# Optimization experiments

Hardware: AMD Instinct MI355X
Metric: run time of the kernel (lower is better)

The kernel has to match this reference:

```python
import jax, jax.numpy as jnp
import numpy as np

H = 16        # num_heads
NB = 64       # n_buckets
NH = 6        # n_hyperplanes = log2(NB)


def setup_inputs() -> dict:
    key = jax.random.key(0)
    k = jax.random.split(key, 6)
    E = 1024
    B, S = 2, 2048
    return {
        "x": jax.random.normal(k[0], (B, S, E), jnp.float32),
        "Wq": jax.random.normal(k[1], (E, E), jnp.float32) * (E ** -0.5),
        "bq": jax.random.normal(k[2], (E,), jnp.float32) * 0.02,
        "Wv": jax.random.normal(k[3], (E, E), jnp.float32) * (E ** -0.5),
        "bv": jax.random.normal(k[4], (E,), jnp.float32) * 0.02,
        "hyperplanes": jax.random.normal(k[5], (E // H + 1, NH), jnp.float32),
    }


def reference(x, Wq, bq, Wv, bv, hyperplanes):
    B, S, E = x.shape
    Dh = E // H
    # projections (torch Linear: x @ W.T + b)
    q = (x @ Wq.T + bq).reshape(B, S, H, Dh)
    v = (x @ Wv.T + bv).reshape(B, S, H, Dh)

    # LSH buckets from q: append a ones column, sign-project onto hyperplanes
    qa = jnp.concatenate([q, jnp.ones((B, S, H, 1), q.dtype)], axis=-1)  # [B,S,H,Dh+1]
    proj = jnp.einsum('bshe,en->bshn', qa, hyperplanes)
    bits = (proj >= 0).astype(jnp.int32)
    buckets = jnp.einsum('bshn,n->bsh', bits, 2 ** jnp.arange(NH, dtype=jnp.int32))  # [B,S,H]
    b_hs = buckets.transpose(0, 2, 1)  # [B,H,S]

    q = q.transpose(0, 2, 1, 3)  # [B,H,S,Dh]
    v = v.transpose(0, 2, 1, 3)

    # The original sums, over all NB buckets i, of (q with bucket-i tokens zeroed)
    # times its transpose. Closed form of that sum:
    #   sum_i (1-d[bs,i])(1-d[bt,i]) = NB - 2 + [bs == bt]
    scores = jnp.einsum('bhsd,bhtd->bhst', q, q) / jnp.sqrt(jnp.float32(E))
    same = (b_hs[:, :, :, None] == b_hs[:, :, None, :]).astype(scores.dtype)
    coeff = (NB - 2) + same
    attn = jax.nn.softmax(scores * coeff, axis=-1)  # [B,H,S,S]

    out = jnp.einsum('bhst,bhtd->bhsd', attn, v)
    return out.transpose(0, 2, 1, 3).reshape(B, S, E)
```

## Files before the change

### kernel.cpp

```cpp
#include <hip/hip_runtime.h>


typedef short short8 __attribute__((ext_vector_type(8)));
typedef float f32x4 __attribute__((ext_vector_type(4)));
typedef unsigned short us4 __attribute__((ext_vector_type(4)));

__device__ __forceinline__ float bff(unsigned short h) {
    return __uint_as_float(((unsigned int)h) << 16);
}
__device__ __forceinline__ unsigned short f2bf(float f) {
    unsigned int u = __float_as_uint(f);
    u += 0x7fffu + ((u >> 16) & 1u);
    return (unsigned short)(u >> 16);
}

__device__ __forceinline__ void glds16(const unsigned short* g, unsigned short* l) {
    __builtin_amdgcn_global_load_lds(
        (const __attribute__((address_space(1))) unsigned int*)g,
        (__attribute__((address_space(3))) unsigned int*)l, 16, 0, 0);
}

__global__ __launch_bounds__(256) void split_all(
    const float* __restrict__ x, const float* __restrict__ Wq,
    const float* __restrict__ Wv,
    unsigned short* __restrict__ xh, unsigned short* __restrict__ xl,
    unsigned short* __restrict__ Wqh, unsigned short* __restrict__ Wql,
    unsigned short* __restrict__ Wvh)
{
    const int blk = blockIdx.x;
    const float* in;
    unsigned short *hi, *lo;
    int idx;
    if (blk < 4096) {
        idx = blk * 256 + threadIdx.x; in = x; hi = xh; lo = xl;
    } else if (blk < 5120) {
        idx = (blk - 4096) * 256 + threadIdx.x; in = Wq; hi = Wqh; lo = Wql;
    } else {
        idx = (blk - 5120) * 256 + threadIdx.x; in = Wv; hi = Wvh; lo = nullptr;
    }
    const float4 v = ((const float4*)in)[idx];
    us4 h;
    h.x = f2bf(v.x); h.y = f2bf(v.y); h.z = f2bf(v.z); h.w = f2bf(v.w);
    ((us4*)hi)[idx] = h;
    if (lo) {
        us4 l;
        l.x = f2bf(v.x - bff(h.x)); l.y = f2bf(v.y - bff(h.y));
        l.z = f2bf(v.z - bff(h.z)); l.w = f2bf(v.w - bff(h.w));
        ((us4*)lo)[idx] = l;
    }
}

__global__ __launch_bounds__(256, 1) void gemm_qv(
    const unsigned short* __restrict__ xh, const unsigned short* __restrict__ xl,
    const unsigned short* __restrict__ wqh, const unsigned short* __restrict__ wql,
    const unsigned short* __restrict__ wvh,
    const float* __restrict__ bq, const float* __restrict__ bv,
    float* __restrict__ Qf, unsigned short* __restrict__ Qb,
    unsigned short* __restrict__ Qlo, unsigned short* __restrict__ Vt)
{
    __shared__ unsigned short Ah[128 * 64], Al[128 * 64];
    __shared__ unsigned short Bh[128 * 64], Bl[128 * 64];

    const int tid = threadIdx.x;
    const int w = tid >> 6, lane = tid & 63;
    const int i = lane & 15, qd = lane >> 4;
    const int l8 = lane >> 3, j = lane & 7;
    const int nw = w * 32;
    const int blk = blockIdx.x;
    const bool isq = blk < 256;

    f32x4 acc[8][2];
#pragma unroll
    for (int a = 0; a < 8; ++a)
#pragma unroll
        for (int b2 = 0; b2 < 2; ++b2) acc[a][b2] = f32x4{0.f, 0.f, 0.f, 0.f};

    const int gro = ((j ^ l8) << 3);

    if (isq) {
        const int m0 = (blk >> 3) * 128;
        const int n0 = (blk & 7) * 128;
        for (int k0 = 0; k0 < 1024; k0 += 64) {
            __syncthreads();
#pragma unroll
            for (int c = 0; c < 4; ++c) {
                const int r = w * 32 + c * 8;
                const size_t gx = (size_t)(m0 + r + l8) * 1024 + k0 + gro;
                const size_t gw = (size_t)(n0 + r + l8) * 1024 + k0 + gro;
                glds16(xh + gx, &Ah[r * 64]);
                glds16(xl + gx, &Al[r * 64]);
                glds16(wqh + gw, &Bh[r * 64]);
                glds16(wql + gw, &Bl[r * 64]);
            }
            __syncthreads();
#pragma unroll
            for (int kc = 0; kc < 2; ++kc) {
                const int ch = (((kc * 4 + qd) ^ (i & 7)) << 3);
                short8 ah[8], al[8], bh2[2], bl2[2];
#pragma unroll
                for (int mm = 0; mm < 8; ++mm) {
                    ah[mm] = *(const short8*)&Ah[(mm * 16 + i) * 64 + ch];
                    al[mm] = *(const short8*)&Al[(mm * 16 + i) * 64 + ch];
                }
#pragma unroll
                for (int nn = 0; nn < 2; ++nn) {
                    bh2[nn] = *(const short8*)&Bh[(nw + nn * 16 + i) * 64 + ch];
                    bl2[nn] = *(const short8*)&Bl[(nw + nn * 16 + i) * 64 + ch];
                }
#pragma unroll
                for (int mm = 0; mm < 8; ++mm)
#pragma unroll
                    for (int nn = 0; nn < 2; ++nn) {
                        acc[mm][nn] = __builtin_amdgcn_mfma_f32_16x16x32_bf16(
                            ah[mm], bh2[nn], acc[mm][nn], 0, 0, 0);
                        acc[mm][nn] = __builtin_amdgcn_mfma_f32_16x16x32_bf16(
                            al[mm], bh2[nn], acc[mm][nn], 0, 0, 0);
                        acc[mm][nn] = __builtin_amdgcn_mfma_f32_16x16x32_bf16(
                            ah[mm], bl2[nn], acc[mm][nn], 0, 0, 0);
                    }
            }
        }
#pragma unroll
        for (int mm = 0; mm < 8; ++mm)
#pragma unroll
            for (int nn = 0; nn < 2; ++nn)
#pragma unroll
                for (int rr = 0; rr < 4; ++rr) {
                    const int row = m0 + mm * 16 + qd * 4 + rr;
                    const int col = n0 + nw + nn * 16 + i;
                    const float v = acc[mm][nn][rr] + bq[col];
                    Qf[(size_t)row * 1024 + col] = v;
                    const unsigned short hs = f2bf(v);
                    const float lo = v - bff(hs);
                    const int b = row >> 11, s = row & 2047;
                    const int hh = col >> 6, d = col & 63;
                    const size_t oi = ((size_t)((b << 4) + hh) * 2048 + s) * 64 + d;
                    Qb[oi] = hs;
                    Qlo[oi] = f2bf(lo);
                }
    } else {
        const int b2 = blk - 256;
        const int m0 = (b2 & 7) * 128;
        const int n0 = (b2 >> 3) * 128;
        for (int k0 = 0; k0 < 1024; k0 += 64) {
            __syncthreads();
#pragma unroll
            for (int c = 0; c < 4; ++c) {
                const int r = w * 32 + c * 8;
                glds16(wvh + (size_t)(m0 + r + l8) * 1024 + k0 + gro, &Ah[r * 64]);
                glds16(xh + (size_t)(n0 + r + l8) * 1024 + k0 + gro, &Bh[r * 64]);
            }
            __syncthreads();
#pragma unroll
            for (int kc = 0; kc < 2; ++kc) {
                const int ch = (((kc * 4 + qd) ^ (i & 7)) << 3);
                short8 af[8], bf2[2];
#pragma unroll
                for (int mm = 0; mm < 8; ++mm)
                    af[mm] = *(const short8*)&Ah[(mm * 16 + i) * 64 + ch];
#pragma unroll
                for (int nn = 0; nn < 2; ++nn)
                    bf2[nn] = *(const short8*)&Bh[(nw + nn * 16 + i) * 64 + ch];
#pragma unroll
                for (int mm = 0; mm < 8; ++mm)
#pragma unroll
                    for (int nn = 0; nn < 2; ++nn)
                        acc[mm][nn] = __builtin_amdgcn_mfma_f32_16x16x32_bf16(
                            af[mm], bf2[nn], acc[mm][nn], 0, 0, 0);
            }
        }
#pragma unroll
        for (int mm = 0; mm < 8; ++mm)
#pragma unroll
            for (int nn = 0; nn < 2; ++nn)
#pragma unroll
                for (int rr = 0; rr < 4; ++rr) {
                    const int rch = m0 + mm * 16 + qd * 4 + rr;
                    const int tok = n0 + nw + nn * 16 + i;
                    const float v = acc[mm][nn][rr] + bv[rch];
                    const int b = tok >> 11, s = tok & 2047;
                    Vt[((size_t)(b * 1024 + rch)) * 2048 + s] = f2bf(v);
                }
    }
}

__global__ __launch_bounds__(256) void bucket_kernel(
    const float* __restrict__ Qf, const float* __restrict__ hp,
    int* __restrict__ buckets, float* __restrict__ rown)
{
    __shared__ float hpl[65 * 6];
    const int tid = threadIdx.x;
    if (tid < 65 * 6) hpl[tid] = hp[tid];
    __syncthreads();

    const int idx = blockIdx.x * 256 + tid;
    const int m = idx >> 4, h = idx & 15;
    const float4* q4 = (const float4*)(Qf + (size_t)m * 1024 + h * 64);

    float pj[6];
    float nrm = 0.f;
#pragma unroll
    for (int n = 0; n < 6; ++n) pj[n] = hpl[64 * 6 + n];
    for (int d4 = 0; d4 < 16; ++d4) {
        const float4 qv = q4[d4];
        nrm = fmaf(qv.x, qv.x, nrm); nrm = fmaf(qv.y, qv.y, nrm);
        nrm = fmaf(qv.z, qv.z, nrm); nrm = fmaf(qv.w, qv.w, nrm);
#pragma unroll
        for (int n = 0; n < 6; ++n) {
            pj[n] = fmaf(qv.x, hpl[(d4 * 4 + 0) * 6 + n], pj[n]);
            pj[n] = fmaf(qv.y, hpl[(d4 * 4 + 1) * 6 + n], pj[n]);
            pj[n] = fmaf(qv.z, hpl[(d4 * 4 + 2) * 6 + n], pj[n]);
            pj[n] = fmaf(qv.w, hpl[(d4 * 4 + 3) * 6 + n], pj[n]);
        }
    }
    int bkt = 0;
#pragma unroll
    for (int n = 0; n < 6; ++n) bkt |= (pj[n] >= 0.f) << n;
    const int off = ((m >> 11) * 16 + h) * 2048 + (m & 2047);
    buckets[off] = bkt;
    rown[off] = nrm;
}

__global__ __launch_bounds__(256, 2) void attn_kernel(
    const unsigned short* __restrict__ Qb, const unsigned short* __restrict__ Qlo,
    const unsigned short* __restrict__ Vt, const int* __restrict__ bks,
    const float* __restrict__ rown, float* __restrict__ out)
{
    __shared__ unsigned short Khi[2][64 * 64];
    __shared__ unsigned short Klo[2][64 * 64];
    __shared__ unsigned short Vs[2][64 * 64];
    __shared__ unsigned short P[4][16 * 64];
    __shared__ float smax[4];

    const int tid = threadIdx.x;
    const int w = tid >> 6, lane = tid & 63;
    const int i = lane & 15, qd = lane >> 4;
    const int l8 = lane >> 3, j = lane & 7;
    const int bh = blockIdx.x;
    const int qbase = blockIdx.y * 128 + w * 32;

    const unsigned short* Qh = Qb + (size_t)bh * 2048 * 64;
    const unsigned short* Ql = Qlo + (size_t)bh * 2048 * 64;
    const unsigned short* Vb = Vt + (size_t)bh * 64 * 2048;
    const int* bk = bks + bh * 2048;
    const float* rnh = rown + bh * 2048;
    unsigned short* Pw = &P[w][0];

    float lm = 0.f;
    for (int t = tid; t < 2048; t += 256) lm = fmaxf(lm, rnh[t]);
#pragma unroll
    for (int msk = 1; msk < 64; msk <<= 1) lm = fmaxf(lm, __shfl_xor(lm, msk));
    if (lane == 0) smax[w] = lm;
    __syncthreads();
    const float sqM = sqrtf(fmaxf(fmaxf(smax[0], smax[1]),
                                  fmaxf(smax[2], smax[3])));

    float m2row[2][4], lrun[2][4];
    int qbr[2][4];
#pragma unroll
    for (int ms = 0; ms < 2; ++ms)
#pragma unroll
        for (int r = 0; r < 4; ++r) {
            const int row = qbase + ms * 16 + qd * 4 + r;
            m2row[ms][r] = 2.84030586f * sqrtf(rnh[row]) * sqM + 0.72134754f;
            qbr[ms][r] = bk[row];
            lrun[ms][r] = 0.f;
        }

    short8 aqh0[2], aqh1[2], aql0[2], aql1[2];
#pragma unroll
    for (int ms = 0; ms < 2; ++ms) {
        const unsigned short* qp = Qh + (size_t)(qbase + ms * 16 + i) * 64 + qd * 8;
        const unsigned short* lp = Ql + (size_t)(qbase + ms * 16 + i) * 64 + qd * 8;
        aqh0[ms] = *(const short8*)qp; aqh1[ms] = *(const short8*)(qp + 32);
        aql0[ms] = *(const short8*)lp; aql1[ms] = *(const short8*)(lp + 32);
    }

    f32x4 o[2][4];
#pragma unroll
    for (int ms = 0; ms < 2; ++ms)
#pragma unroll
        for (int d = 0; d < 4; ++d) o[ms][d] = f32x4{0.f, 0.f, 0.f, 0.f};

    const int swz = ((j ^ l8) << 3);

#pragma unroll
    for (int c2 = 0; c2 < 2; ++c2) {
        const int r = w * 16 + c2 * 8 + l8;
        glds16(Qh + (size_t)r * 64 + swz, &Khi[0][w * 1024 + c2 * 512]);
        glds16(Ql + (size_t)r * 64 + swz, &Klo[0][w * 1024 + c2 * 512]);
        glds16(Vb + (size_t)r * 2048 + swz, &Vs[0][w * 1024 + c2 * 512]);
    }

    for (int it = 0; it < 32; ++it) {
        const int t0 = it * 64;
        const int cur = it & 1;
        __syncthreads();
        if (it < 31) {
            const int t0n = t0 + 64;
            const int nxt = cur ^ 1;
#pragma unroll
            for (int c2 = 0; c2 < 2; ++c2) {
                const int r = w * 16 + c2 * 8 + l8;
                glds16(Qh + (size_t)(t0n + r) * 64 + swz, &Khi[nxt][w * 1024 + c2 * 512]);
                glds16(Ql + (size_t)(t0n + r) * 64 + swz, &Klo[nxt][w * 1024 + c2 * 512]);
                glds16(Vb + (size_t)r * 2048 + t0n + swz, &Vs[nxt][w * 1024 + c2 * 512]);
            }
        }

        f32x4 s[2][4];
        int kb[4];
#pragma unroll
        for (int sub = 0; sub < 4; ++sub) {
            const int kr = sub * 16 + i;
            const int sw = i & 7;
            const short8 bh0 = *(const short8*)&Khi[cur][kr * 64 + ((qd ^ sw) << 3)];
            const short8 bh1 = *(const short8*)&Khi[cur][kr * 64 + (((qd + 4) ^ sw) << 3)];
            const short8 bl0 = *(const short8*)&Klo[cur][kr * 64 + ((qd ^ sw) << 3)];
            const short8 bl1 = *(const short8*)&Klo[cur][kr * 64 + (((qd + 4) ^ sw) << 3)];
            kb[sub] = bk[t0 + kr];
#pragma unroll
            for (int ms = 0; ms < 2; ++ms) {
                f32x4 t = f32x4{0.f, 0.f, 0.f, 0.f};
                t = __builtin_amdgcn_mfma_f32_16x16x32_bf16(aqh0[ms], bh0, t, 0, 0, 0);
                t = __builtin_amdgcn_mfma_f32_16x16x32_bf16(aqh1[ms], bh1, t, 0, 0, 0);
                t = __builtin_amdgcn_mfma_f32_16x16x32_bf16(aql0[ms], bh0, t, 0, 0, 0);
                t = __builtin_amdgcn_mfma_f32_16x16x32_bf16(aql1[ms], bh1, t, 0, 0, 0);
                t = __builtin_amdgcn_mfma_f32_16x16x32_bf16(aqh0[ms], bl0, t, 0, 0, 0);
                t = __builtin_amdgcn_mfma_f32_16x16x32_bf16(aqh1[ms], bl1, t, 0, 0, 0);
                s[ms][sub] = t;
            }
        }

        short8 vb0[4], vb1[4];
#pragma unroll
        for (int dsub = 0; dsub < 4; ++dsub) {
            const int dr = dsub * 16 + i;
            const int sw = i & 7;
            vb0[dsub] = *(const short8*)&Vs[cur][dr * 64 + ((qd ^ sw) << 3)];
            vb1[dsub] = *(const short8*)&Vs[cur][dr * 64 + (((qd + 4) ^ sw) << 3)];
        }

#pragma unroll
        for (int ms = 0; ms < 2; ++ms) {
#pragma unroll
            for (int sub = 0; sub < 4; ++sub)
#pragma unroll
                for (int r = 0; r < 4; ++r) {
                    const float c2f = (kb[sub] == qbr[ms][r]) ? 2.84030586f
                                                              : 2.79522164f;
                    const float p = exp2f(fmaf(s[ms][sub][r], c2f, -m2row[ms][r]));
                    lrun[ms][r] += p;
                    const unsigned int pu = __float_as_uint(p);
                    const int row = qd * 4 + r, col = sub * 16 + i;
                    Pw[row * 64 + (((col >> 3) ^ (row & 7)) << 3) + (col & 7)] =
                        (unsigned short)(pu >> 16);
                }
            const short8 pa0 = *(const short8*)&Pw[i * 64 + ((qd ^ (i & 7)) << 3)];
            const short8 pa1 = *(const short8*)&Pw[i * 64 + (((qd + 4) ^ (i & 7)) << 3)];
#pragma unroll
            for (int dsub = 0; dsub < 4; ++dsub) {
                o[ms][dsub] = __builtin_amdgcn_mfma_f32_16x16x32_bf16(
                    pa0, vb0[dsub], o[ms][dsub], 0, 0, 0);
                o[ms][dsub] = __builtin_amdgcn_mfma_f32_16x16x32_bf16(
                    pa1, vb1[dsub], o[ms][dsub], 0, 0, 0);
            }
        }
    }

#pragma unroll
    for (int ms = 0; ms < 2; ++ms)
#pragma unroll
        for (int r = 0; r < 4; ++r) {
#pragma unroll
            for (int msk = 1; msk < 16; msk <<= 1)
                lrun[ms][r] += __shfl_xor(lrun[ms][r], msk);
        }
    const int b = bh >> 4, h = bh & 15;
#pragma unroll
    for (int ms = 0; ms < 2; ++ms)
#pragma unroll
        for (int dsub = 0; dsub < 4; ++dsub)
#pragma unroll
            for (int r = 0; r < 4; ++r) {
                const float v = o[ms][dsub][r] / lrun[ms][r];
                const int srow = qbase + ms * 16 + qd * 4 + r;
                out[((size_t)(b * 2048 + srow)) * 1024 + h * 64 + dsub * 16 + i] = v;
            }
}

extern "C" void kernel_launch(void* const* d_in, const int* in_sizes, int n_in,
                              void* d_out, int out_size, void* d_ws, size_t ws_size,
                              hipStream_t stream)
{
    const float* x  = (const float*)d_in[0];
    const float* Wq = (const float*)d_in[1];
    const float* bq = (const float*)d_in[2];
    const float* Wv = (const float*)d_in[3];
    const float* bv = (const float*)d_in[4];
    const float* hp = (const float*)d_in[5];
    float* out = (float*)d_out;

    char* ws = (char*)d_ws;
    const size_t MB = (size_t)1 << 20;
    unsigned short* xh  = (unsigned short*)(ws);
    unsigned short* xl  = (unsigned short*)(ws + 8 * MB);
    unsigned short* Wqh = (unsigned short*)(ws + 16 * MB);
    unsigned short* Wql = (unsigned short*)(ws + 18 * MB);
    unsigned short* Wvh = (unsigned short*)(ws + 20 * MB);
    unsigned short* Qb  = (unsigned short*)(ws + 22 * MB);
    unsigned short* Qlo = (unsigned short*)(ws + 30 * MB);
    unsigned short* Vt  = (unsigned short*)(ws + 38 * MB);
    float*          Qf  = (float*)(ws + 46 * MB);
    int*        buckets = (int*)(ws + 62 * MB);
    float*         rown = (float*)(ws + 62 * MB + 256 * 1024);

    split_all<<<dim3(6144), 256, 0, stream>>>(x, Wq, Wv, xh, xl, Wqh, Wql, Wvh);
    gemm_qv<<<dim3(512), 256, 0, stream>>>(xh, xl, Wqh, Wql, Wvh, bq, bv,
                                           Qf, Qb, Qlo, Vt);
    bucket_kernel<<<dim3(256), 256, 0, stream>>>(Qf, hp, buckets, rown);
    attn_kernel<<<dim3(32, 16), 256, 0, stream>>>(Qb, Qlo, Vt, buckets, rown, out);
}
```

Measured before the change: 229.5 us.

## Shrink attention tile to 16 rows per wave and drop double buffering

Each wave in the attention kernel now handles 16 query rows instead of 32, and the grid doubles to 32x32 blocks. The K/V LDS tiles become single-buffered with two barriers per iteration, and launch bounds rise to 4 blocks per CU. The aim is more resident waves and lower register and LDS use so the scheduler can hide latency. The cost is that each K/V tile loaded is reused across half as many query rows, which doubles global and LDS traffic, and the copy of the next tile no longer overlaps compute.

```diff
diff --git a/kernel.cpp b/kernel.cpp
--- a/kernel.cpp
+++ b/kernel.cpp
@@ -221,14 +221,14 @@
     rown[off] = nrm;
 }
 
-__global__ __launch_bounds__(256, 2) void attn_kernel(
+__global__ __launch_bounds__(256, 4) void attn_kernel(
     const unsigned short* __restrict__ Qb, const unsigned short* __restrict__ Qlo,
     const unsigned short* __restrict__ Vt, const int* __restrict__ bks,
     const float* __restrict__ rown, float* __restrict__ out)
 {
-    __shared__ unsigned short Khi[2][64 * 64];
-    __shared__ unsigned short Klo[2][64 * 64];
-    __shared__ unsigned short Vs[2][64 * 64];
+    __shared__ unsigned short Khi[64 * 64];
+    __shared__ unsigned short Klo[64 * 64];
+    __shared__ unsigned short Vs[64 * 64];
     __shared__ unsigned short P[4][16 * 64];
     __shared__ float smax[4];
 
@@ -237,7 +237,7 @@
     const int i = lane & 15, qd = lane >> 4;
     const int l8 = lane >> 3, j = lane & 7;
     const int bh = blockIdx.x;
-    const int qbase = blockIdx.y * 128 + w * 32;
+    const int qbase = blockIdx.y * 64 + w * 16;
 
     const unsigned short* Qh = Qb + (size_t)bh * 2048 * 64;
     const unsigned short* Ql = Qlo + (size_t)bh * 2048 * 64;
@@ -255,81 +255,59 @@
     const float sqM = sqrtf(fmaxf(fmaxf(smax[0], smax[1]),
                                   fmaxf(smax[2], smax[3])));
 
-    float m2row[2][4], lrun[2][4];
-    int qbr[2][4];
-#pragma unroll
-    for (int ms = 0; ms < 2; ++ms)
-#pragma unroll
-        for (int r = 0; r < 4; ++r) {
-            const int row = qbase + ms * 16 + qd * 4 + r;
-            m2row[ms][r] = 2.84030586f * sqrtf(rnh[row]) * sqM + 0.72134754f;
-            qbr[ms][r] = bk[row];
-            lrun[ms][r] = 0.f;
-        }
-
-    short8 aqh0[2], aqh1[2], aql0[2], aql1[2];
-#pragma unroll
-    for (int ms = 0; ms < 2; ++ms) {
-        const unsigned short* qp = Qh + (size_t)(qbase + ms * 16 + i) * 64 + qd * 8;
-        const unsigned short* lp = Ql + (size_t)(qbase + ms * 16 + i) * 64 + qd * 8;
-        aqh0[ms] = *(const short8*)qp; aqh1[ms] = *(const short8*)(qp + 32);
-        aql0[ms] = *(const short8*)lp; aql1[ms] = *(const short8*)(lp + 32);
-    }
-
-    f32x4 o[2][4];
-#pragma unroll
-    for (int ms = 0; ms < 2; ++ms)
-#pragma unroll
-        for (int d = 0; d < 4; ++d) o[ms][d] = f32x4{0.f, 0.f, 0.f, 0.f};
-
-    const int swz = ((j ^ l8) << 3);
-
-#pragma unroll
-    for (int c2 = 0; c2 < 2; ++c2) {
-        const int r = w * 16 + c2 * 8 + l8;
-        glds16(Qh + (size_t)r * 64 + swz, &Khi[0][w * 1024 + c2 * 512]);
-        glds16(Ql + (size_t)r * 64 + swz, &Klo[0][w * 1024 + c2 * 512]);
-        glds16(Vb + (size_t)r * 2048 + swz, &Vs[0][w * 1024 + c2 * 512]);
-    }
-
-    for (int it = 0; it < 32; ++it) {
-        const int t0 = it * 64;
-        const int cur = it & 1;
+    float m2row[4], lrun[4];
+    int qbr[4];
+#pragma unroll
+    for (int r = 0; r < 4; ++r) {
+        const int row = qbase + qd * 4 + r;
+        m2row[r] = 2.84030586f * sqrtf(rnh[row]) * sqM + 0.72134754f;
+        qbr[r] = bk[row];
+        lrun[r] = 0.f;
+    }
+
+    short8 aqh0, aqh1, aql0, aql1;
+    {
+        const unsigned short* qp = Qh + (size_t)(qbase + i) * 64 + qd * 8;
+        const unsigned short* lp = Ql + (size_t)(qbase + i) * 64 + qd * 8;
+        aqh0 = *(const short8*)qp; aqh1 = *(const short8*)(qp + 32);
+        aql0 = *(const short8*)lp; aql1 = *(const short8*)(lp + 32);
+    }
+
+    f32x4 o[4];
+#pragma unroll
+    for (int d = 0; d < 4; ++d) o[d] = f32x4{0.f, 0.f, 0.f, 0.f};
+
+    for (int t0 = 0; t0 < 2048; t0 += 64) {
         __syncthreads();
-        if (it < 31) {
-            const int t0n = t0 + 64;
-            const int nxt = cur ^ 1;
-#pragma unroll
-            for (int c2 = 0; c2 < 2; ++c2) {
-                const int r = w * 16 + c2 * 8 + l8;
-                glds16(Qh + (size_t)(t0n + r) * 64 + swz, &Khi[nxt][w * 1024 + c2 * 512]);
-                glds16(Ql + (size_t)(t0n + r) * 64 + swz, &Klo[nxt][w * 1024 + c2 * 512]);
-                glds16(Vb + (size_t)r * 2048 + t0n + swz, &Vs[nxt][w * 1024 + c2 * 512]);
-            }
-        }
-
-        f32x4 s[2][4];
+#pragma unroll
+        for (int c2 = 0; c2 < 2; ++c2) {
+            const int r = w * 16 + c2 * 8 + l8;
+            const int swz = ((j ^ l8) << 3);
+            glds16(Qh + (size_t)(t0 + r) * 64 + swz, &Khi[w * 1024 + c2 * 512]);
+            glds16(Ql + (size_t)(t0 + r) * 64 + swz, &Klo[w * 1024 + c2 * 512]);
+            glds16(Vb + (size_t)r * 2048 + t0 + swz, &Vs[w * 1024 + c2 * 512]);
+        }
+        __syncthreads();
+
+        f32x4 s[4];
         int kb[4];
 #pragma unroll
         for (int sub = 0; sub < 4; ++sub) {
             const int kr = sub * 16 + i;
             const int sw = i & 7;
-            const short8 bh0 = *(const short8*)&Khi[cur][kr * 64 + ((qd ^ sw) << 3)];
-            const short8 bh1 = *(const short8*)&Khi[cur][kr * 64 + (((qd + 4) ^ sw) << 3)];
-            const short8 bl0 = *(const short8*)&Klo[cur][kr * 64 + ((qd ^ sw) << 3)];
-            const short8 bl1 = *(const short8*)&Klo[cur][kr * 64 + (((qd + 4) ^ sw) << 3)];
+            const short8 bh0 = *(const short8*)&Khi[kr * 64 + ((qd ^ sw) << 3)];
+            const short8 bh1 = *(const short8*)&Khi[kr * 64 + (((qd + 4) ^ sw) << 3)];
+            const short8 bl0 = *(const short8*)&Klo[kr * 64 + ((qd ^ sw) << 3)];
+            const short8 bl1 = *(const short8*)&Klo[kr * 64 + (((qd + 4) ^ sw) << 3)];
             kb[sub] = bk[t0 + kr];
-#pragma unroll
-            for (int ms = 0; ms < 2; ++ms) {
-                f32x4 t = f32x4{0.f, 0.f, 0.f, 0.f};
-                t = __builtin_amdgcn_mfma_f32_16x16x32_bf16(aqh0[ms], bh0, t, 0, 0, 0);
-                t = __builtin_amdgcn_mfma_f32_16x16x32_bf16(aqh1[ms], bh1, t, 0, 0, 0);
-                t = __builtin_amdgcn_mfma_f32_16x16x32_bf16(aql0[ms], bh0, t, 0, 0, 0);
-                t = __builtin_amdgcn_mfma_f32_16x16x32_bf16(aql1[ms], bh1, t, 0, 0, 0);
-                t = __builtin_amdgcn_mfma_f32_16x16x32_bf16(aqh0[ms], bl0, t, 0, 0, 0);
-                t = __builtin_amdgcn_mfma_f32_16x16x32_bf16(aqh1[ms], bl1, t, 0, 0, 0);
-                s[ms][sub] = t;
-            }
+            f32x4 t = f32x4{0.f, 0.f, 0.f, 0.f};
+            t = __builtin_amdgcn_mfma_f32_16x16x32_bf16(aqh0, bh0, t, 0, 0, 0);
+            t = __builtin_amdgcn_mfma_f32_16x16x32_bf16(aqh1, bh1, t, 0, 0, 0);
+            t = __builtin_amdgcn_mfma_f32_16x16x32_bf16(aql0, bh0, t, 0, 0, 0);
+            t = __builtin_amdgcn_mfma_f32_16x16x32_bf16(aql1, bh1, t, 0, 0, 0);
+            t = __builtin_amdgcn_mfma_f32_16x16x32_bf16(aqh0, bl0, t, 0, 0, 0);
+            t = __builtin_amdgcn_mfma_f32_16x16x32_bf16(aqh1, bl1, t, 0, 0, 0);
+            s[sub] = t;
         }
 
         short8 vb0[4], vb1[4];
@@ -337,56 +315,49 @@
         for (int dsub = 0; dsub < 4; ++dsub) {
             const int dr = dsub * 16 + i;
             const int sw = i & 7;
-            vb0[dsub] = *(const short8*)&Vs[cur][dr * 64 + ((qd ^ sw) << 3)];
-            vb1[dsub] = *(const short8*)&Vs[cur][dr * 64 + (((qd + 4) ^ sw) << 3)];
-        }
-
-#pragma unroll
-        for (int ms = 0; ms < 2; ++ms) {
-#pragma unroll
-            for (int sub = 0; sub < 4; ++sub)
-#pragma unroll
-                for (int r = 0; r < 4; ++r) {
-                    const float c2f = (kb[sub] == qbr[ms][r]) ? 2.84030586f
-                                                              : 2.79522164f;
-                    const float p = exp2f(fmaf(s[ms][sub][r], c2f, -m2row[ms][r]));
-                    lrun[ms][r] += p;
-                    const unsigned int pu = __float_as_uint(p);
-                    const int row = qd * 4 + r, col = sub * 16 + i;
-                    Pw[row * 64 + (((col >> 3) ^ (row & 7)) << 3) + (col & 7)] =
-                        (unsigned short)(pu >> 16);
-                }
-            const short8 pa0 = *(const short8*)&Pw[i * 64 + ((qd ^ (i & 7)) << 3)];
-            const short8 pa1 = *(const short8*)&Pw[i * 64 + (((qd + 4) ^ (i & 7)) << 3)];
-#pragma unroll
-            for (int dsub = 0; dsub < 4; ++dsub) {
-                o[ms][dsub] = __builtin_amdgcn_mfma_f32_16x16x32_bf16(
-                    pa0, vb0[dsub], o[ms][dsub], 0, 0, 0);
-                o[ms][dsub] = __builtin_amdgcn_mfma_f32_16x16x32_bf16(
-                    pa1, vb1[dsub], o[ms][dsub], 0, 0, 0);
-            }
-        }
-    }
-
-#pragma unroll
-    for (int ms = 0; ms < 2; ++ms)
+            vb0[dsub] = *(const short8*)&Vs[dr * 64 + ((qd ^ sw) << 3)];
+            vb1[dsub] = *(const short8*)&Vs[dr * 64 + (((qd + 4) ^ sw) << 3)];
+        }
+
+#pragma unroll
+        for (int sub = 0; sub < 4; ++sub)
+#pragma unroll
+            for (int r = 0; r < 4; ++r) {
+                const float c2f = (kb[sub] == qbr[r]) ? 2.84030586f
+                                                      : 2.79522164f;
+                const float p = exp2f(fmaf(s[sub][r], c2f, -m2row[r]));
+                lrun[r] += p;
+                const unsigned int pu = __float_as_uint(p);
+                const int row = qd * 4 + r, col = sub * 16 + i;
+                Pw[row * 64 + (((col >> 3) ^ (row & 7)) << 3) + (col & 7)] =
+                    (unsigned short)(pu >> 16);
+            }
+        const short8 pa0 = *(const short8*)&Pw[i * 64 + ((qd ^ (i & 7)) << 3)];
+        const short8 pa1 = *(const short8*)&Pw[i * 64 + (((qd + 4) ^ (i & 7)) << 3)];
+#pragma unroll
+        for (int dsub = 0; dsub < 4; ++dsub) {
+            o[dsub] = __builtin_amdgcn_mfma_f32_16x16x32_bf16(
+                pa0, vb0[dsub], o[dsub], 0, 0, 0);
+            o[dsub] = __builtin_amdgcn_mfma_f32_16x16x32_bf16(
+                pa1, vb1[dsub], o[dsub], 0, 0, 0);
+        }
+    }
+
+#pragma unroll
+    for (int r = 0; r < 4; ++r) {
+#pragma unroll
+        for (int msk = 1; msk < 16; msk <<= 1)
+            lrun[r] += __shfl_xor(lrun[r], msk);
+    }
+    const int b = bh >> 4, h = bh & 15;
+#pragma unroll
+    for (int dsub = 0; dsub < 4; ++dsub)
 #pragma unroll
         for (int r = 0; r < 4; ++r) {
-#pragma unroll
-            for (int msk = 1; msk < 16; msk <<= 1)
-                lrun[ms][r] += __shfl_xor(lrun[ms][r], msk);
-        }
-    const int b = bh >> 4, h = bh & 15;
-#pragma unroll
-    for (int ms = 0; ms < 2; ++ms)
-#pragma unroll
-        for (int dsub = 0; dsub < 4; ++dsub)
-#pragma unroll
-            for (int r = 0; r < 4; ++r) {
-                const float v = o[ms][dsub][r] / lrun[ms][r];
-                const int srow = qbase + ms * 16 + qd * 4 + r;
-                out[((size_t)(b * 2048 + srow)) * 1024 + h * 64 + dsub * 16 + i] = v;
-            }
+            const float v = o[dsub][r] / lrun[r];
+            const int srow = qbase + qd * 4 + r;
+            out[((size_t)(b * 2048 + srow)) * 1024 + h * 64 + dsub * 16 + i] = v;
+        }
 }
 
 extern "C" void kernel_launch(void* const* d_in, const int* in_sizes, int n_in,
@@ -419,5 +390,5 @@
     gemm_qv<<<dim3(512), 256, 0, stream>>>(xh, xl, Wqh, Wql, Wvh, bq, bv,
                                            Qf, Qb, Qlo, Vt);
     bucket_kernel<<<dim3(256), 256, 0, stream>>>(Qf, hp, buckets, rown);
-    attn_kernel<<<dim3(32, 16), 256, 0, stream>>>(Qb, Qlo, Vt, buckets, rown, out);
-}
+    attn_kernel<<<dim3(32, 32), 256, 0, stream>>>(Qb, Qlo, Vt, buckets, rown, out);
+}
```

Result: slower. 247.1 us (+7.7%).

## Replace double-buffered prefetch with synchronous 128-key tile load per iteration

Applied to the files above, without the earlier changes.

Removes the software-pipelined double buffer: each iteration now loads two 64-key halves into both LDS buffers, waits on a barrier, then computes both halves. This halves the number of loop iterations and barrier pairs per key, but global loads no longer overlap with MFMA compute. Latency hiding must now come from other resident waves.

```diff
diff --git a/kernel.cpp b/kernel.cpp
--- a/kernel.cpp
+++ b/kernel.cpp
@@ -284,86 +284,82 @@
 
     const int swz = ((j ^ l8) << 3);
 
-#pragma unroll
-    for (int c2 = 0; c2 < 2; ++c2) {
-        const int r = w * 16 + c2 * 8 + l8;
-        glds16(Qh + (size_t)r * 64 + swz, &Khi[0][w * 1024 + c2 * 512]);
-        glds16(Ql + (size_t)r * 64 + swz, &Klo[0][w * 1024 + c2 * 512]);
-        glds16(Vb + (size_t)r * 2048 + swz, &Vs[0][w * 1024 + c2 * 512]);
-    }
-
-    for (int it = 0; it < 32; ++it) {
-        const int t0 = it * 64;
-        const int cur = it & 1;
+    for (int t0 = 0; t0 < 2048; t0 += 128) {
         __syncthreads();
-        if (it < 31) {
-            const int t0n = t0 + 64;
-            const int nxt = cur ^ 1;
+#pragma unroll
+        for (int hf = 0; hf < 2; ++hf) {
+            const int t0h = t0 + hf * 64;
 #pragma unroll
             for (int c2 = 0; c2 < 2; ++c2) {
                 const int r = w * 16 + c2 * 8 + l8;
-                glds16(Qh + (size_t)(t0n + r) * 64 + swz, &Khi[nxt][w * 1024 + c2 * 512]);
-                glds16(Ql + (size_t)(t0n + r) * 64 + swz, &Klo[nxt][w * 1024 + c2 * 512]);
-                glds16(Vb + (size_t)r * 2048 + t0n + swz, &Vs[nxt][w * 1024 + c2 * 512]);
-            }
-        }
-
-        f32x4 s[2][4];
-        int kb[4];
-#pragma unroll
-        for (int sub = 0; sub < 4; ++sub) {
-            const int kr = sub * 16 + i;
-            const int sw = i & 7;
-            const short8 bh0 = *(const short8*)&Khi[cur][kr * 64 + ((qd ^ sw) << 3)];
-            const short8 bh1 = *(const short8*)&Khi[cur][kr * 64 + (((qd + 4) ^ sw) << 3)];
-            const short8 bl0 = *(const short8*)&Klo[cur][kr * 64 + ((qd ^ sw) << 3)];
-            const short8 bl1 = *(const short8*)&Klo[cur][kr * 64 + (((qd + 4) ^ sw) << 3)];
-            kb[sub] = bk[t0 + kr];
+                glds16(Qh + (size_t)(t0h + r) * 64 + swz, &Khi[hf][w * 1024 + c2 * 512]);
+                glds16(Ql + (size_t)(t0h + r) * 64 + swz, &Klo[hf][w * 1024 + c2 * 512]);
+                glds16(Vb + (size_t)r * 2048 + t0h + swz, &Vs[hf][w * 1024 + c2 * 512]);
+            }
+        }
+        __syncthreads();
+
+#pragma unroll
+        for (int hf = 0; hf < 2; ++hf) {
+            const int t0h = t0 + hf * 64;
+
+            f32x4 s[2][4];
+            int kb[4];
+#pragma unroll
+            for (int sub = 0; sub < 4; ++sub) {
+                const int kr = sub * 16 + i;
+                const int sw = i & 7;
+                const short8 bh0 = *(const short8*)&Khi[hf][kr * 64 + ((qd ^ sw) << 3)];
+                const short8 bh1 = *(const short8*)&Khi[hf][kr * 64 + (((qd + 4) ^ sw) << 3)];
+                const short8 bl0 = *(const short8*)&Klo[hf][kr * 64 + ((qd ^ sw) << 3)];
+                const short8 bl1 = *(const short8*)&Klo[hf][kr * 64 + (((qd + 4) ^ sw) << 3)];
+                kb[sub] = bk[t0h + kr];
+#pragma unroll
+                for (int ms = 0; ms < 2; ++ms) {
+                    f32x4 t = f32x4{0.f, 0.f, 0.f, 0.f};
+                    t = __builtin_amdgcn_mfma_f32_16x16x32_bf16(aqh0[ms], bh0, t, 0, 0, 0);
+                    t = __builtin_amdgcn_mfma_f32_16x16x32_bf16(aqh1[ms], bh1, t, 0, 0, 0);
+                    t = __builtin_amdgcn_mfma_f32_16x16x32_bf16(aql0[ms], bh0, t, 0, 0, 0);
+                    t = __builtin_amdgcn_mfma_f32_16x16x32_bf16(aql1[ms], bh1, t, 0, 0, 0);
+                    t = __builtin_amdgcn_mfma_f32_16x16x32_bf16(aqh0[ms], bl0, t, 0, 0, 0);
+                    t = __builtin_amdgcn_mfma_f32_16x16x32_bf16(aqh1[ms], bl1, t, 0, 0, 0);
+                    s[ms][sub] = t;
+                }
+            }
+
+            short8 vb0[4], vb1[4];
+#pragma unroll
+            for (int dsub = 0; dsub < 4; ++dsub) {
+                const int dr = dsub * 16 + i;
+                const int sw = i & 7;
+                vb0[dsub] = *(const short8*)&Vs[hf][dr * 64 + ((qd ^ sw) << 3)];
+                vb1[dsub] = *(const short8*)&Vs[hf][dr * 64 + (((qd + 4) ^ sw) << 3)];
+            }
+
 #pragma unroll
             for (int ms = 0; ms < 2; ++ms) {
-                f32x4 t = f32x4{0.f, 0.f, 0.f, 0.f};
-                t = __builtin_amdgcn_mfma_f32_16x16x32_bf16(aqh0[ms], bh0, t, 0, 0, 0);
-                t = __builtin_amdgcn_mfma_f32_16x16x32_bf16(aqh1[ms], bh1, t, 0, 0, 0);
-                t = __builtin_amdgcn_mfma_f32_16x16x32_bf16(aql0[ms], bh0, t, 0, 0, 0);
-                t = __builtin_amdgcn_mfma_f32_16x16x32_bf16(aql1[ms], bh1, t, 0, 0, 0);
-                t = __builtin_amdgcn_mfma_f32_16x16x32_bf16(aqh0[ms], bl0, t, 0, 0, 0);
-                t = __builtin_amdgcn_mfma_f32_16x16x32_bf16(aqh1[ms], bl1, t, 0, 0, 0);
-                s[ms][sub] = t;
-            }
-        }
-
-        short8 vb0[4], vb1[4];
-#pragma unroll
-        for (int dsub = 0; dsub < 4; ++dsub) {
-            const int dr = dsub * 16 + i;
-            const int sw = i & 7;
-            vb0[dsub] = *(const short8*)&Vs[cur][dr * 64 + ((qd ^ sw) << 3)];
-            vb1[dsub] = *(const short8*)&Vs[cur][dr * 64 + (((qd + 4) ^ sw) << 3)];
-        }
-
-#pragma unroll
-        for (int ms = 0; ms < 2; ++ms) {
-#pragma unroll
-            for (int sub = 0; sub < 4; ++sub)
-#pragma unroll
-                for (int r = 0; r < 4; ++r) {
-                    const float c2f = (kb[sub] == qbr[ms][r]) ? 2.84030586f
-                                                              : 2.79522164f;
-                    const float p = exp2f(fmaf(s[ms][sub][r], c2f, -m2row[ms][r]));
-                    lrun[ms][r] += p;
-                    const unsigned int pu = __float_as_uint(p);
-                    const int row = qd * 4 + r, col = sub * 16 + i;
-                    Pw[row * 64 + (((col >> 3) ^ (row & 7)) << 3) + (col & 7)] =
-                        (unsigned short)(pu >> 16);
-                }
-            const short8 pa0 = *(const short8*)&Pw[i * 64 + ((qd ^ (i & 7)) << 3)];
-            const short8 pa1 = *(const short8*)&Pw[i * 64 + (((qd + 4) ^ (i & 7)) << 3)];
-#pragma unroll
-            for (int dsub = 0; dsub < 4; ++dsub) {
-                o[ms][dsub] = __builtin_amdgcn_mfma_f32_16x16x32_bf16(
-                    pa0, vb0[dsub], o[ms][dsub], 0, 0, 0);
-                o[ms][dsub] = __builtin_amdgcn_mfma_f32_16x16x32_bf16(
-                    pa1, vb1[dsub], o[ms][dsub], 0, 0, 0);
+#pragma unroll
+                for (int sub = 0; sub < 4; ++sub)
+#pragma unroll
+                    for (int r = 0; r < 4; ++r) {
+                        const float c2f = (kb[sub] == qbr[ms][r]) ? 2.84030586f
+                                                                  : 2.79522164f;
+                        const float p = exp2f(fmaf(s[ms][sub][r], c2f, -m2row[ms][r]));
+                        lrun[ms][r] += p;
+                        const unsigned int pu = __float_as_uint(p);
+                        const int row = qd * 4 + r, col = sub * 16 + i;
+                        Pw[row * 64 + (((col >> 3) ^ (row & 7)) << 3) + (col & 7)] =
+                            (unsigned short)(pu >> 16);
+                    }
+                const short8 pa0 = *(const short8*)&Pw[i * 64 + ((qd ^ (i & 7)) << 3)];
+                const short8 pa1 = *(const short8*)&Pw[i * 64 + (((qd + 4) ^ (i & 7)) << 3)];
+#pragma unroll
+                for (int dsub = 0; dsub < 4; ++dsub) {
+                    o[ms][dsub] = __builtin_amdgcn_mfma_f32_16x16x32_bf16(
+                        pa0, vb0[dsub], o[ms][dsub], 0, 0, 0);
+                    o[ms][dsub] = __builtin_amdgcn_mfma_f32_16x16x32_bf16(
+                        pa1, vb1[dsub], o[ms][dsub], 0, 0, 0);
+                }
             }
         }
     }
```

After: 221.7 us. 3.4% less time.
